# Performance work log

Measured on AMD Instinct MI355X. Metric: run time of the kernel, lower is better.

Reference implementation:

```python
import jax, jax.numpy as jnp
import numpy as np

B, T, C, K, V = 4, 4096, 128, 64, 64
EPS = 1e-5


def layer_norm(x, g, b):
    mu = jnp.mean(x, axis=-1, keepdims=True)
    var = jnp.var(x, axis=-1, keepdims=True)
    return (x - mu) * jax.lax.rsqrt(var + EPS) * g + b


def setup_inputs() -> dict:
    key = jax.random.key(0)
    ks = jax.random.split(key, 8)
    s = 1.0 / np.sqrt(C)
    return {
        "x": jax.random.normal(ks[0], (B, T, C), dtype=jnp.float32),
        "Wq": jax.random.uniform(ks[1], (C, K), jnp.float32, -s, s),
        "bq": jnp.zeros((K,), jnp.float32),
        "Wk": jax.random.uniform(ks[2], (C, K), jnp.float32, -s, s),
        "bk": jnp.zeros((K,), jnp.float32),
        "Wv": jax.random.uniform(ks[3], (C, V), jnp.float32, -s, s),
        "bv": jnp.zeros((V,), jnp.float32),
        "gq": jnp.ones((K,), jnp.float32), "bgq": jnp.zeros((K,), jnp.float32),
        "gk": jnp.ones((K,), jnp.float32), "bgk": jnp.zeros((K,), jnp.float32),
        "gv": jnp.ones((V,), jnp.float32), "bgv": jnp.zeros((V,), jnp.float32),
        "go": jnp.ones((V,), jnp.float32), "bgo": jnp.zeros((V,), jnp.float32),
    }


def reference(x, Wq, bq, Wk, bk, Wv, bv, gq, bgq, gk, bgk, gv, bgv, go, bgo):
    # projections: B x T x {K,K,V}
    q = layer_norm(x @ Wq + bq, gq, bgq)
    k = layer_norm(x @ Wk + bk, gk, bgk)
    v = layer_norm(x @ Wv + bv, gv, bgv)
    sqrt_k = jnp.asarray(np.sqrt(K), x.dtype)
    # full B x T x T causal score matrix (faithful to the original bmm+mask)
    logits = jnp.einsum("btk,bsk->bts", q, k) / sqrt_k
    t = jnp.arange(T)
    causal = t[:, None] >= t[None, :]  # lower-triangular incl. diagonal
    logits = jnp.where(causal[None], logits, -jnp.inf)
    probs = jax.nn.softmax(logits, axis=-1)
    read = jnp.einsum("bts,bsv->btv", probs, v)
    read = layer_norm(read, go, bgo)
    return jnp.concatenate([x, read], axis=2)  # B x T x (C+V)
```

## Files before the change

kernel.cpp:

```cpp
#include <hip/hip_runtime.h>

#define TT 4096

typedef unsigned short u16;
typedef unsigned int u32;

typedef short bf16x8 __attribute__((ext_vector_type(8)));
typedef float f32x4 __attribute__((ext_vector_type(4)));

union U8 {
  uint2 q[2];
  uint4 u4;
  bf16x8 v;
  short s[8];
};

static __device__ __forceinline__ u16 f2bf(float f) {
  union { float f; u32 u; } cv;
  cv.f = f;
  u32 r = cv.u + 0x7FFFu + ((cv.u >> 16) & 1u);
  return (u16)(r >> 16);
}
static __device__ __forceinline__ u32 pk2(float a, float b) {
  return (u32)f2bf(a) | ((u32)f2bf(b) << 16);
}
static __device__ __forceinline__ float bf2f(u16 h) {
  union { u32 u; float f; } cv;
  cv.u = ((u32)h) << 16;
  return cv.f;
}

__global__ __launch_bounds__(64)
void wpack(const float* __restrict__ Wq, const float* __restrict__ Wk,
           const float* __restrict__ Wv, u16* __restrict__ wf)
{
  const int g = blockIdx.x;
  const int p = g >> 4, s = (g >> 2) & 3, nt = g & 3;
  const int l = threadIdx.x, lg = l >> 4, l15 = l & 15;
  const float* W = (p == 0) ? Wq : (p == 1) ? Wk : Wv;
  const int n = l15 + 16 * nt;
  U8 o;
#pragma unroll
  for (int j = 0; j < 8; ++j) {
    int k = 32 * s + ((j < 4) ? (4 * lg + j) : (16 + 4 * lg + (j - 4)));
    o.s[j] = (short)f2bf(W[k * 64 + n]);
  }
  *(uint4*)(wf + (size_t)(g * 64 + l) * 8) = o.u4;
}

__global__ __launch_bounds__(256)
void proj_mfma(const float* __restrict__ x, const u16* __restrict__ wf,
               const float* __restrict__ bq, const float* __restrict__ bk,
               const float* __restrict__ bv,
               const float* __restrict__ gq, const float* __restrict__ bgq,
               const float* __restrict__ gk, const float* __restrict__ bgk,
               const float* __restrict__ gv, const float* __restrict__ bgv,
               u16* __restrict__ qo, u16* __restrict__ ko, u16* __restrict__ vto,
               float* __restrict__ out)
{
  __shared__ u16 xs[64 * 128];
  const int bx = blockIdx.x;
  const int xcd = bx & 7, i = bx >> 3;
  const int tile = xcd * 32 + (i & 31);
  const int p = i >> 5;
  const int rowbase = tile * 64;
  const int t = threadIdx.x;

  {
    const int row = t >> 2, seg = t & 3;
    const float4* src = (const float4*)(x + (size_t)(rowbase + row) * 128 + seg * 32);
    float4 f[8];
#pragma unroll
    for (int q = 0; q < 8; ++q) f[q] = src[q];
    if ((p == 0 && seg < 2) || (p == 1 && seg >= 2)) {
      float4* dst = (float4*)(out + (size_t)(rowbase + row) * 192 + seg * 32);
#pragma unroll
      for (int q = 0; q < 8; ++q) dst[q] = f[q];
    }
    const int base = row * 256 + seg * 64;
    const int swz = (row & 7) << 4;
    char* xb = (char*)xs;
#pragma unroll
    for (int q = 0; q < 4; ++q) {
      uint4 u;
      u.x = pk2(f[2 * q].x, f[2 * q].y);
      u.y = pk2(f[2 * q].z, f[2 * q].w);
      u.z = pk2(f[2 * q + 1].x, f[2 * q + 1].y);
      u.w = pk2(f[2 * q + 1].z, f[2 * q + 1].w);
      *(uint4*)(xb + ((base + 16 * q) ^ swz)) = u;
    }
  }

  const int w = t >> 6, l = t & 63, lg = l >> 4, l15 = l & 15;
  U8 bfr[4][4];
  const u16* wp = wf + (size_t)p * (16 * 64 * 8);
#pragma unroll
  for (int s = 0; s < 4; ++s)
#pragma unroll
    for (int nt = 0; nt < 4; ++nt)
      bfr[s][nt].u4 = *(const uint4*)(wp + ((s * 4 + nt) * 64 + l) * 8);

  __syncthreads();

  f32x4 acc[4];
#pragma unroll
  for (int nt = 0; nt < 4; ++nt) acc[nt] = (f32x4){0.f, 0.f, 0.f, 0.f};
  const int abase = (16 * w + l15) * 256;
  const int aswz = (l15 & 7) << 4;
  const char* xb = (const char*)xs;
#pragma unroll
  for (int s = 0; s < 4; ++s) {
    U8 af;
    af.q[0] = *(const uint2*)(xb + ((abase + s * 64 + 8 * lg) ^ aswz));
    af.q[1] = *(const uint2*)(xb + ((abase + s * 64 + 8 * lg + 32) ^ aswz));
#pragma unroll
    for (int nt = 0; nt < 4; ++nt)
      acc[nt] = __builtin_amdgcn_mfma_f32_16x16x32_bf16(af.v, bfr[s][nt].v, acc[nt], 0, 0, 0);
  }

  const float* bb = (p == 0) ? bq : (p == 1) ? bk : bv;
  const float* gg = (p == 0) ? gq : (p == 1) ? gk : gv;
  const float* hh = (p == 0) ? bgq : (p == 1) ? bgk : bgv;
  float bcol[4], gcol[4], hcol[4];
#pragma unroll
  for (int nt = 0; nt < 4; ++nt) {
    int col = l15 + 16 * nt;
    bcol[nt] = bb[col]; gcol[nt] = gg[col]; hcol[nt] = hh[col];
  }
  float vals[4][4];
#pragma unroll
  for (int nt = 0; nt < 4; ++nt)
#pragma unroll
    for (int r = 0; r < 4; ++r) vals[nt][r] = acc[nt][r] + bcol[nt];

  float s1[4], s2[4];
#pragma unroll
  for (int r = 0; r < 4; ++r) {
    s1[r] = vals[0][r] + vals[1][r] + vals[2][r] + vals[3][r];
    s2[r] = vals[0][r] * vals[0][r] + vals[1][r] * vals[1][r]
          + vals[2][r] * vals[2][r] + vals[3][r] * vals[3][r];
#pragma unroll
    for (int d = 1; d < 16; d <<= 1) {
      s1[r] += __shfl_xor(s1[r], d);
      s2[r] += __shfl_xor(s2[r], d);
    }
  }

  if (p < 2) {
    u16* dst = (p == 0) ? qo : ko;
#pragma unroll
    for (int r = 0; r < 4; ++r) {
      float mu = s1[r] * (1.f / 64.f);
      float var = s2[r] * (1.f / 64.f) - mu * mu;
      float rs = rsqrtf(var + 1e-5f);
      int grow = rowbase + 16 * w + 4 * lg + r;
#pragma unroll
      for (int nt = 0; nt < 4; ++nt)
        dst[(size_t)grow * 64 + l15 + 16 * nt] =
            f2bf((vals[nt][r] - mu) * rs * gcol[nt] + hcol[nt]);
    }
  } else {
    const int b = rowbase >> 12;
    const int tl0 = (rowbase & 4095) + 16 * w + 4 * lg;
#pragma unroll
    for (int r = 0; r < 4; ++r) {
      float mu = s1[r] * (1.f / 64.f);
      float var = s2[r] * (1.f / 64.f) - mu * mu;
      float rs = rsqrtf(var + 1e-5f);
#pragma unroll
      for (int nt = 0; nt < 4; ++nt)
        vto[(size_t)(b * 64 + l15 + 16 * nt) * TT + tl0 + r] =
            f2bf((vals[nt][r] - mu) * rs * gcol[nt] + hcol[nt]);
    }
  }
}

__global__ __launch_bounds__(256)
void attn_splitW(const u16* __restrict__ qg, const u16* __restrict__ kg,
                 const u16* __restrict__ vtg,
                 float* __restrict__ mP, float* __restrict__ lP,
                 u16* __restrict__ aP,
                 int Wseg, int maxseg, int halfcnt)
{
  __shared__ u16 kl[64 * 64];
  __shared__ u16 vl[64 * 64];
  const int bx = blockIdx.x;
  const int xcd = bx & 7, b = xcd >> 1, e = xcd & 1;
  const int j = e * halfcnt + (bx >> 3);
  const int Wh = Wseg >> 1;
  int Q = 0;
  while (Wh * (Q + 1) * (Q + 2) <= j) ++Q;
  const int ip = j - Wh * Q * (Q + 1);
  const int dv = ip / (Q + 1);
  const int q = Wseg * Q + dv;
  const int s = ip - dv * (Q + 1);
  const int q0 = q * 64;
  const int tileid = b * 64 + q;
  const int it0 = s * Wseg;
  const int it1 = min(it0 + Wseg, q + 1);

  const int t = threadIdx.x;
  const int w = t >> 6, l = t & 63;
  const int l15 = l & 15, lg = l >> 4;
  const int swzl = (l15 & 7) << 4;

  const int qrow = q0 + 16 * w + l15;
  const u16* qrp = qg + (size_t)(b * TT + qrow) * 64;
  U8 qf[2];
#pragma unroll
  for (int hh = 0; hh < 2; ++hh) {
    qf[hh].q[0] = *(const uint2*)(qrp + 32 * hh + 4 * lg);
    qf[hh].q[1] = *(const uint2*)(qrp + 32 * hh + 4 * lg + 16);
  }

  const int key = t >> 2;
  const int part = t & 3;
  const int sbase = key * 128 + part * 32;
  const int ssw = (key & 7) << 4;
  uint4 kr0, kr1, vr0, vr1;
  {
    const u16* ks = kg + (size_t)(b * TT + it0 * 64 + key) * 64 + part * 16;
    kr0 = ((const uint4*)ks)[0];
    kr1 = ((const uint4*)ks)[1];
    const u16* vs = vtg + (size_t)(b * 64 + key) * TT + it0 * 64 + part * 16;
    vr0 = ((const uint4*)vs)[0];
    vr1 = ((const uint4*)vs)[1];
  }

  float m_run = -1e30f, l_run = 0.f;
  f32x4 acc[4];
#pragma unroll
  for (int ct = 0; ct < 4; ++ct) acc[ct] = (f32x4){0.f, 0.f, 0.f, 0.f};

  for (int it = it0; it < it1; ++it) {
    const int kb = it * 64;
    {
      char* kd = (char*)kl;
      char* vd = (char*)vl;
      *(uint4*)(kd + ((sbase + 0) ^ ssw)) = kr0;
      *(uint4*)(kd + ((sbase + 16) ^ ssw)) = kr1;
      *(uint4*)(vd + ((sbase + 0) ^ ssw)) = vr0;
      *(uint4*)(vd + ((sbase + 16) ^ ssw)) = vr1;
    }
    __syncthreads();
    if (it + 1 < it1) {
      const u16* ks = kg + (size_t)(b * TT + (it + 1) * 64 + key) * 64 + part * 16;
      kr0 = ((const uint4*)ks)[0];
      kr1 = ((const uint4*)ks)[1];
      const u16* vs = vtg + (size_t)(b * 64 + key) * TT + (it + 1) * 64 + part * 16;
      vr0 = ((const uint4*)vs)[0];
      vr1 = ((const uint4*)vs)[1];
    }

    f32x4 st[4];
#pragma unroll
    for (int t4 = 0; t4 < 4; ++t4) {
      const int rbase = (16 * t4 + l15) * 128 + 8 * lg;
      const char* kp = (const char*)kl;
      U8 kf0, kf1;
      kf0.q[0] = *(const uint2*)(kp + ((rbase + 0) ^ swzl));
      kf0.q[1] = *(const uint2*)(kp + ((rbase + 32) ^ swzl));
      kf1.q[0] = *(const uint2*)(kp + ((rbase + 64) ^ swzl));
      kf1.q[1] = *(const uint2*)(kp + ((rbase + 96) ^ swzl));
      f32x4 d = {0.f, 0.f, 0.f, 0.f};
      d = __builtin_amdgcn_mfma_f32_16x16x32_bf16(kf0.v, qf[0].v, d, 0, 0, 0);
      d = __builtin_amdgcn_mfma_f32_16x16x32_bf16(kf1.v, qf[1].v, d, 0, 0, 0);
      st[t4] = d;
    }

    float sv[16];
    const bool needmask = (kb + 63 > q0 + 16 * w);
#pragma unroll
    for (int t4 = 0; t4 < 4; ++t4) {
#pragma unroll
      for (int r = 0; r < 4; ++r) {
        float sc = st[t4][r] * 0.125f;
        if (needmask) {
          int keyidx = kb + 16 * t4 + 4 * lg + r;
          if (keyidx > qrow) sc = -1e30f;
        }
        sv[t4 * 4 + r] = sc;
      }
    }
    float mt = sv[0];
#pragma unroll
    for (int i = 1; i < 16; ++i) mt = fmaxf(mt, sv[i]);
    mt = fmaxf(mt, __shfl_xor(mt, 16));
    mt = fmaxf(mt, __shfl_xor(mt, 32));
    const float mnew = fmaxf(m_run, mt);
    const float al = __expf(m_run - mnew);
    float pv[16];
    float rsum = 0.f;
#pragma unroll
    for (int i = 0; i < 16; ++i) { pv[i] = __expf(sv[i] - mnew); rsum += pv[i]; }
    rsum += __shfl_xor(rsum, 16);
    rsum += __shfl_xor(rsum, 32);
    l_run = l_run * al + rsum;
    m_run = mnew;
    float ar[4];
#pragma unroll
    for (int r = 0; r < 4; ++r) ar[r] = __shfl(al, 4 * lg + r);
#pragma unroll
    for (int ct = 0; ct < 4; ++ct) {
#pragma unroll
      for (int r = 0; r < 4; ++r) acc[ct][r] *= ar[r];
    }
    U8 pa[2];
#pragma unroll
    for (int u = 0; u < 2; ++u) {
#pragma unroll
      for (int i = 0; i < 8; ++i) pa[u].s[i] = (short)f2bf(pv[8 * u + i]);
    }

#pragma unroll
    for (int ct = 0; ct < 4; ++ct) {
      const int vb = (16 * ct + l15) * 128 + 8 * lg;
      const char* vp = (const char*)vl;
#pragma unroll
      for (int u = 0; u < 2; ++u) {
        U8 vf;
        vf.q[0] = *(const uint2*)(vp + ((vb + 64 * u + 0) ^ swzl));
        vf.q[1] = *(const uint2*)(vp + ((vb + 64 * u + 32) ^ swzl));
        acc[ct] = __builtin_amdgcn_mfma_f32_16x16x32_bf16(pa[u].v, vf.v, acc[ct], 0, 0, 0);
      }
    }
    __syncthreads();
  }

  const size_t pbase = (size_t)(tileid * maxseg + s) * 64;
  if (lg == 0) {
    mP[pbase + 16 * w + l15] = m_run;
    lP[pbase + 16 * w + l15] = l_run;
  }
#pragma unroll
  for (int ct = 0; ct < 4; ++ct) {
#pragma unroll
    for (int r = 0; r < 4; ++r) {
      int rin = 16 * w + 4 * lg + r;
      aP[(pbase + rin) * 64 + l15 + 16 * ct] = f2bf(acc[ct][r]);
    }
  }
}

__global__ __launch_bounds__(256)
void attn_mergeW(const float* __restrict__ mP, const float* __restrict__ lP,
                 const u16* __restrict__ aP,
                 const float* __restrict__ go, const float* __restrict__ bgo,
                 float* __restrict__ out, int jshift, int maxseg)
{
  const int t = threadIdx.x;
  const int w = t >> 6, c = t & 63;
  const int row = blockIdx.x * 4 + w;
  const int tid2 = row >> 6, rin = row & 63;
  const int q = tid2 & 63;
  const int ns = (q >> jshift) + 1;

  float m = -1e30f, L = 0.f, o = 0.f;
  for (int s = 0; s < ns; ++s) {
    const size_t pbase = (size_t)(tid2 * maxseg + s) * 64;
    float ms = mP[pbase + rin];
    float ls = lP[pbase + rin];
    float a = bf2f(aP[(pbase + rin) * 64 + c]);
    float mn = fmaxf(m, ms);
    float w0 = __expf(m - mn), w1 = __expf(ms - mn);
    L = L * w0 + ls * w1;
    o = o * w0 + a * w1;
    m = mn;
  }
  o /= L;

  float s1 = o, s2 = o * o;
#pragma unroll
  for (int d = 1; d < 64; d <<= 1) {
    s1 += __shfl_xor(s1, d);
    s2 += __shfl_xor(s2, d);
  }
  float mu = s1 * (1.f / 64.f);
  float var = s2 * (1.f / 64.f) - mu * mu;
  float rs = rsqrtf(var + 1e-5f);
  out[(size_t)row * 192 + 128 + c] = (o - mu) * rs * go[c] + bgo[c];
}

__global__ __launch_bounds__(128)
void attn1(const u16* __restrict__ qg, const u16* __restrict__ kg,
           const u16* __restrict__ vtg,
           const float* __restrict__ go, const float* __restrict__ bgo,
           float* __restrict__ out)
{
  __shared__ u16 kl[64 * 64];
  __shared__ u16 vl[64 * 64];
  const int bx = blockIdx.x;
  const int tt = (bx < 256) ? bx : (767 - bx);
  const int b = tt >> 7;
  const int q0 = (tt & 127) * 32;
  const int tid = threadIdx.x;
  const int w = tid >> 6;
  const int l = tid & 63;
  const int l15 = l & 15;
  const int lg = l >> 4;
  const int swzl = (l15 & 7) << 4;

  const int qrow = q0 + 16 * w + l15;
  const u16* qrp = qg + (size_t)(b * TT + qrow) * 64;
  U8 qf[2];
#pragma unroll
  for (int h = 0; h < 2; ++h) {
    qf[h].q[0] = *(const uint2*)(qrp + 32 * h + 4 * lg);
    qf[h].q[1] = *(const uint2*)(qrp + 32 * h + 4 * lg + 16);
  }

  float m_run = -1e30f, l_run = 0.f;
  f32x4 acc[4];
#pragma unroll
  for (int ct = 0; ct < 4; ++ct) acc[ct] = (f32x4){0.f, 0.f, 0.f, 0.f};

  const int nkv = (q0 >> 6) + 1;
  for (int it = 0; it < nkv; ++it) {
    const int kb = it * 64;
    {
      const int key = tid >> 1;
      const int dh = (tid & 1) * 32;
      const u16* ks = kg + (size_t)(b * TT + kb + key) * 64 + dh;
      uint4 d0 = *(const uint4*)(ks + 0);
      uint4 d1 = *(const uint4*)(ks + 8);
      uint4 d2 = *(const uint4*)(ks + 16);
      uint4 d3 = *(const uint4*)(ks + 24);
      const int base = key * 128 + dh * 2;
      const int sw = (key & 7) << 4;
      char* kd = (char*)kl;
      *(uint4*)(kd + ((base + 0) ^ sw)) = d0;
      *(uint4*)(kd + ((base + 16) ^ sw)) = d1;
      *(uint4*)(kd + ((base + 32) ^ sw)) = d2;
      *(uint4*)(kd + ((base + 48) ^ sw)) = d3;
      const u16* vs = vtg + (size_t)(b * 64 + key) * TT + kb + dh;
      uint4 e0 = *(const uint4*)(vs + 0);
      uint4 e1 = *(const uint4*)(vs + 8);
      uint4 e2 = *(const uint4*)(vs + 16);
      uint4 e3 = *(const uint4*)(vs + 24);
      char* vd = (char*)vl;
      *(uint4*)(vd + ((base + 0) ^ sw)) = e0;
      *(uint4*)(vd + ((base + 16) ^ sw)) = e1;
      *(uint4*)(vd + ((base + 32) ^ sw)) = e2;
      *(uint4*)(vd + ((base + 48) ^ sw)) = e3;
    }
    __syncthreads();

    f32x4 st[4];
#pragma unroll
    for (int t4 = 0; t4 < 4; ++t4) {
      const int rbase = (16 * t4 + l15) * 128 + 8 * lg;
      const char* kp = (const char*)kl;
      U8 kf0, kf1;
      kf0.q[0] = *(const uint2*)(kp + ((rbase + 0) ^ swzl));
      kf0.q[1] = *(const uint2*)(kp + ((rbase + 32) ^ swzl));
      kf1.q[0] = *(const uint2*)(kp + ((rbase + 64) ^ swzl));
      kf1.q[1] = *(const uint2*)(kp + ((rbase + 96) ^ swzl));
      f32x4 d = {0.f, 0.f, 0.f, 0.f};
      d = __builtin_amdgcn_mfma_f32_16x16x32_bf16(kf0.v, qf[0].v, d, 0, 0, 0);
      d = __builtin_amdgcn_mfma_f32_16x16x32_bf16(kf1.v, qf[1].v, d, 0, 0, 0);
      st[t4] = d;
    }

    float sv[16];
    const bool needmask = (kb + 63 > q0 + 16 * w);
#pragma unroll
    for (int t4 = 0; t4 < 4; ++t4) {
#pragma unroll
      for (int r = 0; r < 4; ++r) {
        float sc = st[t4][r] * 0.125f;
        if (needmask) {
          int keyidx = kb + 16 * t4 + 4 * lg + r;
          if (keyidx > qrow) sc = -1e30f;
        }
        sv[t4 * 4 + r] = sc;
      }
    }
    float mt = sv[0];
#pragma unroll
    for (int i = 1; i < 16; ++i) mt = fmaxf(mt, sv[i]);
    mt = fmaxf(mt, __shfl_xor(mt, 16));
    mt = fmaxf(mt, __shfl_xor(mt, 32));
    const float mnew = fmaxf(m_run, mt);
    const float al = __expf(m_run - mnew);
    float p[16];
    float rsum = 0.f;
#pragma unroll
    for (int i = 0; i < 16; ++i) { p[i] = __expf(sv[i] - mnew); rsum += p[i]; }
    rsum += __shfl_xor(rsum, 16);
    rsum += __shfl_xor(rsum, 32);
    l_run = l_run * al + rsum;
    m_run = mnew;
    float ar[4];
#pragma unroll
    for (int r = 0; r < 4; ++r) ar[r] = __shfl(al, 4 * lg + r);
#pragma unroll
    for (int ct = 0; ct < 4; ++ct) {
#pragma unroll
      for (int r = 0; r < 4; ++r) acc[ct][r] *= ar[r];
    }
    U8 pa[2];
#pragma unroll
    for (int u = 0; u < 2; ++u) {
#pragma unroll
      for (int i = 0; i < 8; ++i) pa[u].s[i] = (short)f2bf(p[8 * u + i]);
    }

#pragma unroll
    for (int ct = 0; ct < 4; ++ct) {
      const int vb = (16 * ct + l15) * 128 + 8 * lg;
      const char* vp = (const char*)vl;
#pragma unroll
      for (int u = 0; u < 2; ++u) {
        U8 vf;
        vf.q[0] = *(const uint2*)(vp + ((vb + 64 * u + 0) ^ swzl));
        vf.q[1] = *(const uint2*)(vp + ((vb + 64 * u + 32) ^ swzl));
        acc[ct] = __builtin_amdgcn_mfma_f32_16x16x32_bf16(pa[u].v, vf.v, acc[ct], 0, 0, 0);
      }
    }
    __syncthreads();
  }

  float linv[4];
#pragma unroll
  for (int r = 0; r < 4; ++r) linv[r] = 1.f / __shfl(l_run, 4 * lg + r);
  float o[4][4];
#pragma unroll
  for (int ct = 0; ct < 4; ++ct) {
#pragma unroll
    for (int r = 0; r < 4; ++r) o[ct][r] = acc[ct][r] * linv[r];
  }
  float s1[4], s2[4];
#pragma unroll
  for (int r = 0; r < 4; ++r) {
    s1[r] = o[0][r] + o[1][r] + o[2][r] + o[3][r];
    s2[r] = o[0][r] * o[0][r] + o[1][r] * o[1][r] + o[2][r] * o[2][r] + o[3][r] * o[3][r];
#pragma unroll
    for (int d = 1; d < 16; d <<= 1) {
      s1[r] += __shfl_xor(s1[r], d);
      s2[r] += __shfl_xor(s2[r], d);
    }
  }
  float gov[4], bgv2[4];
#pragma unroll
  for (int ct = 0; ct < 4; ++ct) {
    gov[ct] = go[16 * ct + l15];
    bgv2[ct] = bgo[16 * ct + l15];
  }
#pragma unroll
  for (int r = 0; r < 4; ++r) {
    float mu = s1[r] * (1.f / 64.f);
    float var = s2[r] * (1.f / 64.f) - mu * mu;
    float rs = rsqrtf(var + 1e-5f);
    int row = q0 + 16 * w + 4 * lg + r;
    float* op = out + (size_t)(b * TT + row) * 192 + 128;
#pragma unroll
    for (int ct = 0; ct < 4; ++ct)
      op[16 * ct + l15] = (o[ct][r] - mu) * rs * gov[ct] + bgv2[ct];
  }
}

extern "C" void kernel_launch(void* const* d_in, const int* in_sizes, int n_in,
                              void* d_out, int out_size, void* d_ws, size_t ws_size,
                              hipStream_t stream) {
  (void)in_sizes; (void)n_in; (void)out_size;
  const float* x   = (const float*)d_in[0];
  const float* Wq  = (const float*)d_in[1];
  const float* bq  = (const float*)d_in[2];
  const float* Wk  = (const float*)d_in[3];
  const float* bk  = (const float*)d_in[4];
  const float* Wv  = (const float*)d_in[5];
  const float* bv  = (const float*)d_in[6];
  const float* gq  = (const float*)d_in[7];
  const float* bgq = (const float*)d_in[8];
  const float* gk  = (const float*)d_in[9];
  const float* bgk = (const float*)d_in[10];
  const float* gv  = (const float*)d_in[11];
  const float* bgv = (const float*)d_in[12];
  const float* go  = (const float*)d_in[13];
  const float* bgo = (const float*)d_in[14];
  float* out = (float*)d_out;

  char* wsb = (char*)d_ws;
  u16* qws  = (u16*)wsb;
  u16* kws  = (u16*)(wsb + (2u << 20));
  u16* vtws = (u16*)(wsb + (4u << 20));
  u16* wfr  = (u16*)(wsb + (6u << 20));
  const size_t OFF_MP = (6u << 20) + 65536;

  wpack<<<48, 64, 0, stream>>>(Wq, Wk, Wv, wfr);
  proj_mfma<<<768, 256, 0, stream>>>(x, wfr, bq, bk, bv,
                                     gq, bgq, gk, bgk, gv, bgv,
                                     qws, kws, vtws, out);

  {
    const size_t MPS8 = 256u * 8 * 64 * 4;
    const size_t APS8 = 256u * 8 * 64 * 64 * 2;
    const size_t OFF_LP8 = OFF_MP + MPS8;
    const size_t OFF_AP8 = OFF_LP8 + MPS8;
    const size_t NEED8 = OFF_AP8 + APS8;
    const size_t MPS32 = 256u * 2 * 64 * 4;
    const size_t APS32 = 256u * 2 * 64 * 64 * 2;
    const size_t OFF_LP32 = OFF_MP + MPS32;
    const size_t OFF_AP32 = OFF_LP32 + MPS32;
    const size_t NEED32 = OFF_AP32 + APS32;

    if (ws_size >= NEED8) {
      float* mP = (float*)(wsb + OFF_MP);
      float* lP = (float*)(wsb + OFF_LP8);
      u16*   aP = (u16*)(wsb + OFF_AP8);
      attn_splitW<<<1152, 256, 0, stream>>>(qws, kws, vtws, mP, lP, aP, 8, 8, 144);
      attn_mergeW<<<4096, 256, 0, stream>>>(mP, lP, aP, go, bgo, out, 3, 8);
    } else if (ws_size >= NEED32) {
      float* mP = (float*)(wsb + OFF_MP);
      float* lP = (float*)(wsb + OFF_LP32);
      u16*   aP = (u16*)(wsb + OFF_AP32);
      attn_splitW<<<384, 256, 0, stream>>>(qws, kws, vtws, mP, lP, aP, 32, 2, 48);
      attn_mergeW<<<4096, 256, 0, stream>>>(mP, lP, aP, go, bgo, out, 5, 2);
    } else {
      attn1<<<512, 128, 0, stream>>>(qws, kws, vtws, go, bgo, out);
    }
  }
}
```

Measured before the change: 72.40 us.

## Load K/V MFMA fragments directly from global, drop LDS staging and barriers

The split-attention kernel no longer stages K and V tiles through shared memory with swizzled writes and two __syncthreads per iteration. Each wave now loads its K and V MFMA fragments straight from global memory, relying on the caches to absorb the fourfold redundant reads across waves. The softmax also moves to the base-2 domain: the log2(e)/8 factor is folded into the score scale and raw v_exp_f32 is used in both split and merge. It also adds a hardware bf16 pack instruction and tree-shaped max and sum reductions. The trade-off is more global and L1 traffic and the loss of the register prefetch of the next tile, in exchange for no LDS round trip and no block-wide synchronisation.

Measured after the change: 186.0 us. +156.9%, slower.

```diff
diff --git a/kernel.cpp b/kernel.cpp
--- a/kernel.cpp
+++ b/kernel.cpp
@@ -13,6 +13,7 @@
   uint4 u4;
   bf16x8 v;
   short s[8];
+  u32 w[4];
 };
 
 static __device__ __forceinline__ u16 f2bf(float f) {
@@ -28,6 +29,12 @@
   union { u32 u; float f; } cv;
   cv.u = ((u32)h) << 16;
   return cv.f;
+}
+static __device__ __forceinline__ float exp2a(float x) {
+  float r; asm("v_exp_f32 %0, %1" : "=v"(r) : "v"(x)); return r;
+}
+static __device__ __forceinline__ u32 cvtpk(float lo, float hi) {
+  u32 r; asm("v_cvt_pk_bf16_f32 %0, %1, %2" : "=v"(r) : "v"(lo), "v"(hi)); return r;
 }
 
 __global__ __launch_bounds__(64)
@@ -176,14 +183,12 @@
 }
 
 __global__ __launch_bounds__(256)
-void attn_splitW(const u16* __restrict__ qg, const u16* __restrict__ kg,
+void attn_splitD(const u16* __restrict__ qg, const u16* __restrict__ kg,
                  const u16* __restrict__ vtg,
                  float* __restrict__ mP, float* __restrict__ lP,
                  u16* __restrict__ aP,
                  int Wseg, int maxseg, int halfcnt)
 {
-  __shared__ u16 kl[64 * 64];
-  __shared__ u16 vl[64 * 64];
   const int bx = blockIdx.x;
   const int xcd = bx & 7, b = xcd >> 1, e = xcd & 1;
   const int j = e * halfcnt + (bx >> 3);
@@ -202,7 +207,6 @@
   const int t = threadIdx.x;
   const int w = t >> 6, l = t & 63;
   const int l15 = l & 15, lg = l >> 4;
-  const int swzl = (l15 & 7) << 4;
 
   const int qrow = q0 + 16 * w + l15;
   const u16* qrp = qg + (size_t)(b * TT + qrow) * 64;
@@ -213,19 +217,13 @@
     qf[hh].q[1] = *(const uint2*)(qrp + 32 * hh + 4 * lg + 16);
   }
 
-  const int key = t >> 2;
-  const int part = t & 3;
-  const int sbase = key * 128 + part * 32;
-  const int ssw = (key & 7) << 4;
-  uint4 kr0, kr1, vr0, vr1;
-  {
-    const u16* ks = kg + (size_t)(b * TT + it0 * 64 + key) * 64 + part * 16;
-    kr0 = ((const uint4*)ks)[0];
-    kr1 = ((const uint4*)ks)[1];
-    const u16* vs = vtg + (size_t)(b * 64 + key) * TT + it0 * 64 + part * 16;
-    vr0 = ((const uint4*)vs)[0];
-    vr1 = ((const uint4*)vs)[1];
-  }
+  const u16* kp = kg + (size_t)(b * TT + it0 * 64 + l15) * 64 + 4 * lg;
+  const u16* vp0 = vtg + (size_t)(b * 64 + l15) * TT + it0 * 64 + 4 * lg;
+  const u16* vp1 = vp0 + (size_t)16 * TT;
+  const u16* vp2 = vp0 + (size_t)32 * TT;
+  const u16* vp3 = vp0 + (size_t)48 * TT;
+
+  const float C = 0.18033688011112042f;
 
   float m_run = -1e30f, l_run = 0.f;
   f32x4 acc[4];
@@ -234,65 +232,77 @@
 
   for (int it = it0; it < it1; ++it) {
     const int kb = it * 64;
-    {
-      char* kd = (char*)kl;
-      char* vd = (char*)vl;
-      *(uint4*)(kd + ((sbase + 0) ^ ssw)) = kr0;
-      *(uint4*)(kd + ((sbase + 16) ^ ssw)) = kr1;
-      *(uint4*)(vd + ((sbase + 0) ^ ssw)) = vr0;
-      *(uint4*)(vd + ((sbase + 16) ^ ssw)) = vr1;
-    }
-    __syncthreads();
-    if (it + 1 < it1) {
-      const u16* ks = kg + (size_t)(b * TT + (it + 1) * 64 + key) * 64 + part * 16;
-      kr0 = ((const uint4*)ks)[0];
-      kr1 = ((const uint4*)ks)[1];
-      const u16* vs = vtg + (size_t)(b * 64 + key) * TT + (it + 1) * 64 + part * 16;
-      vr0 = ((const uint4*)vs)[0];
-      vr1 = ((const uint4*)vs)[1];
+
+    U8 kf[4][2];
+#pragma unroll
+    for (int t4 = 0; t4 < 4; ++t4) {
+#pragma unroll
+      for (int h = 0; h < 2; ++h) {
+        kf[t4][h].q[0] = *(const uint2*)(kp + t4 * 1024 + 32 * h);
+        kf[t4][h].q[1] = *(const uint2*)(kp + t4 * 1024 + 32 * h + 16);
+      }
     }
 
     f32x4 st[4];
 #pragma unroll
     for (int t4 = 0; t4 < 4; ++t4) {
-      const int rbase = (16 * t4 + l15) * 128 + 8 * lg;
-      const char* kp = (const char*)kl;
-      U8 kf0, kf1;
-      kf0.q[0] = *(const uint2*)(kp + ((rbase + 0) ^ swzl));
-      kf0.q[1] = *(const uint2*)(kp + ((rbase + 32) ^ swzl));
-      kf1.q[0] = *(const uint2*)(kp + ((rbase + 64) ^ swzl));
-      kf1.q[1] = *(const uint2*)(kp + ((rbase + 96) ^ swzl));
       f32x4 d = {0.f, 0.f, 0.f, 0.f};
-      d = __builtin_amdgcn_mfma_f32_16x16x32_bf16(kf0.v, qf[0].v, d, 0, 0, 0);
-      d = __builtin_amdgcn_mfma_f32_16x16x32_bf16(kf1.v, qf[1].v, d, 0, 0, 0);
+      d = __builtin_amdgcn_mfma_f32_16x16x32_bf16(kf[t4][0].v, qf[0].v, d, 0, 0, 0);
+      d = __builtin_amdgcn_mfma_f32_16x16x32_bf16(kf[t4][1].v, qf[1].v, d, 0, 0, 0);
       st[t4] = d;
+    }
+
+    U8 vf[4][2];
+#pragma unroll
+    for (int u = 0; u < 2; ++u) {
+      vf[0][u].q[0] = *(const uint2*)(vp0 + 32 * u);
+      vf[0][u].q[1] = *(const uint2*)(vp0 + 32 * u + 16);
+      vf[1][u].q[0] = *(const uint2*)(vp1 + 32 * u);
+      vf[1][u].q[1] = *(const uint2*)(vp1 + 32 * u + 16);
+      vf[2][u].q[0] = *(const uint2*)(vp2 + 32 * u);
+      vf[2][u].q[1] = *(const uint2*)(vp2 + 32 * u + 16);
+      vf[3][u].q[0] = *(const uint2*)(vp3 + 32 * u);
+      vf[3][u].q[1] = *(const uint2*)(vp3 + 32 * u + 16);
     }
 
     float sv[16];
     const bool needmask = (kb + 63 > q0 + 16 * w);
-#pragma unroll
-    for (int t4 = 0; t4 < 4; ++t4) {
-#pragma unroll
-      for (int r = 0; r < 4; ++r) {
-        float sc = st[t4][r] * 0.125f;
-        if (needmask) {
+    if (needmask) {
+#pragma unroll
+      for (int t4 = 0; t4 < 4; ++t4) {
+#pragma unroll
+        for (int r = 0; r < 4; ++r) {
+          float sc = st[t4][r] * C;
           int keyidx = kb + 16 * t4 + 4 * lg + r;
-          if (keyidx > qrow) sc = -1e30f;
+          sv[t4 * 4 + r] = (keyidx > qrow) ? -1e30f : sc;
         }
-        sv[t4 * 4 + r] = sc;
       }
-    }
-    float mt = sv[0];
-#pragma unroll
-    for (int i = 1; i < 16; ++i) mt = fmaxf(mt, sv[i]);
+    } else {
+#pragma unroll
+      for (int t4 = 0; t4 < 4; ++t4) {
+#pragma unroll
+        for (int r = 0; r < 4; ++r) sv[t4 * 4 + r] = st[t4][r] * C;
+      }
+    }
+    float mx[8];
+#pragma unroll
+    for (int i = 0; i < 8; ++i) mx[i] = fmaxf(sv[2 * i], sv[2 * i + 1]);
+#pragma unroll
+    for (int i = 0; i < 4; ++i) mx[i] = fmaxf(mx[2 * i], mx[2 * i + 1]);
+    float mt = fmaxf(fmaxf(mx[0], mx[1]), fmaxf(mx[2], mx[3]));
     mt = fmaxf(mt, __shfl_xor(mt, 16));
     mt = fmaxf(mt, __shfl_xor(mt, 32));
     const float mnew = fmaxf(m_run, mt);
-    const float al = __expf(m_run - mnew);
-    float pv[16];
-    float rsum = 0.f;
-#pragma unroll
-    for (int i = 0; i < 16; ++i) { pv[i] = __expf(sv[i] - mnew); rsum += pv[i]; }
+    const float al = exp2a(m_run - mnew);
+    float p[16];
+#pragma unroll
+    for (int i = 0; i < 16; ++i) p[i] = exp2a(sv[i] - mnew);
+    float sm[8];
+#pragma unroll
+    for (int i = 0; i < 8; ++i) sm[i] = p[2 * i] + p[2 * i + 1];
+#pragma unroll
+    for (int i = 0; i < 4; ++i) sm[i] = sm[2 * i] + sm[2 * i + 1];
+    float rsum = (sm[0] + sm[1]) + (sm[2] + sm[3]);
     rsum += __shfl_xor(rsum, 16);
     rsum += __shfl_xor(rsum, 32);
     l_run = l_run * al + rsum;
@@ -309,22 +319,19 @@
 #pragma unroll
     for (int u = 0; u < 2; ++u) {
 #pragma unroll
-      for (int i = 0; i < 8; ++i) pa[u].s[i] = (short)f2bf(pv[8 * u + i]);
+      for (int k2 = 0; k2 < 4; ++k2)
+        pa[u].w[k2] = cvtpk(p[8 * u + 2 * k2], p[8 * u + 2 * k2 + 1]);
     }
 
 #pragma unroll
     for (int ct = 0; ct < 4; ++ct) {
-      const int vb = (16 * ct + l15) * 128 + 8 * lg;
-      const char* vp = (const char*)vl;
-#pragma unroll
-      for (int u = 0; u < 2; ++u) {
-        U8 vf;
-        vf.q[0] = *(const uint2*)(vp + ((vb + 64 * u + 0) ^ swzl));
-        vf.q[1] = *(const uint2*)(vp + ((vb + 64 * u + 32) ^ swzl));
-        acc[ct] = __builtin_amdgcn_mfma_f32_16x16x32_bf16(pa[u].v, vf.v, acc[ct], 0, 0, 0);
-      }
-    }
-    __syncthreads();
+#pragma unroll
+      for (int u = 0; u < 2; ++u)
+        acc[ct] = __builtin_amdgcn_mfma_f32_16x16x32_bf16(pa[u].v, vf[ct][u].v, acc[ct], 0, 0, 0);
+    }
+
+    kp += 4096;
+    vp0 += 64; vp1 += 64; vp2 += 64; vp3 += 64;
   }
 
   const size_t pbase = (size_t)(tileid * maxseg + s) * 64;
@@ -362,7 +369,7 @@
     float ls = lP[pbase + rin];
     float a = bf2f(aP[(pbase + rin) * 64 + c]);
     float mn = fmaxf(m, ms);
-    float w0 = __expf(m - mn), w1 = __expf(ms - mn);
+    float w0 = exp2a(m - mn), w1 = exp2a(ms - mn);
     L = L * w0 + ls * w1;
     o = o * w0 + a * w1;
     m = mn;
@@ -608,13 +615,13 @@
       float* mP = (float*)(wsb + OFF_MP);
       float* lP = (float*)(wsb + OFF_LP8);
       u16*   aP = (u16*)(wsb + OFF_AP8);
-      attn_splitW<<<1152, 256, 0, stream>>>(qws, kws, vtws, mP, lP, aP, 8, 8, 144);
+      attn_splitD<<<1152, 256, 0, stream>>>(qws, kws, vtws, mP, lP, aP, 8, 8, 144);
       attn_mergeW<<<4096, 256, 0, stream>>>(mP, lP, aP, go, bgo, out, 3, 8);
     } else if (ws_size >= NEED32) {
       float* mP = (float*)(wsb + OFF_MP);
       float* lP = (float*)(wsb + OFF_LP32);
       u16*   aP = (u16*)(wsb + OFF_AP32);
-      attn_splitW<<<384, 256, 0, stream>>>(qws, kws, vtws, mP, lP, aP, 32, 2, 48);
+      attn_splitD<<<384, 256, 0, stream>>>(qws, kws, vtws, mP, lP, aP, 32, 2, 48);
       attn_mergeW<<<4096, 256, 0, stream>>>(mP, lP, aP, go, bgo, out, 5, 2);
     } else {
       attn1<<<512, 128, 0, stream>>>(qws, kws, vtws, go, bgo, out);
```

## Add fixed 4-tile split-K attention kernel with preloaded LDS and lazy rescale

Applied to the files above, without the earlier changes.

Adds a new attention path that splits each query tile's causal key range into segments of four 64-key tiles. Each block preloads all four K/V tiles into swizzled LDS with one barrier, then runs an online softmax. It uses hardware exp2 and packed bf16 conversion, and skips the accumulator rescale unless the max grows past a threshold. A matching merge kernel combines the per-segment partials and applies the output layernorm. This yields more, shorter blocks (2176) for better load balance and fewer syncs, at the cost of more partial-result traffic and a larger workspace.

After: 65.21 us. 1.11x faster.

```diff
diff --git a/kernel.cpp b/kernel.cpp
--- a/kernel.cpp
+++ b/kernel.cpp
@@ -13,6 +13,7 @@
   uint4 u4;
   bf16x8 v;
   short s[8];
+  u32 w[4];
 };
 
 static __device__ __forceinline__ u16 f2bf(float f) {
@@ -28,6 +29,12 @@
   union { u32 u; float f; } cv;
   cv.u = ((u32)h) << 16;
   return cv.f;
+}
+static __device__ __forceinline__ float exp2a(float x) {
+  float r; asm("v_exp_f32 %0, %1" : "=v"(r) : "v"(x)); return r;
+}
+static __device__ __forceinline__ u32 cvtpk(float lo, float hi) {
+  u32 r; asm("v_cvt_pk_bf16_f32 %0, %1, %2" : "=v"(r) : "v"(lo), "v"(hi)); return r;
 }
 
 __global__ __launch_bounds__(64)
@@ -173,6 +180,231 @@
             f2bf((vals[nt][r] - mu) * rs * gcol[nt] + hcol[nt]);
     }
   }
+}
+
+__global__ __launch_bounds__(256)
+void attn_seg4(const u16* __restrict__ qg, const u16* __restrict__ kg,
+               const u16* __restrict__ vtg,
+               float* __restrict__ mP, float* __restrict__ lP,
+               u16* __restrict__ aP)
+{
+  __shared__ u16 kl4[4 * 64 * 64];
+  __shared__ u16 vl4[4 * 64 * 64];
+  const int bx = blockIdx.x;
+  const int xcd = bx & 7, b = xcd >> 1, e = xcd & 1;
+  const int j = e * 272 + (bx >> 3);
+  int Q = 0;
+  while (2 * (Q + 1) * (Q + 2) <= j) ++Q;
+  const int ip = j - 2 * Q * (Q + 1);
+  const int dv = ip / (Q + 1);
+  const int q = 4 * Q + dv;
+  const int s = ip - dv * (Q + 1);
+  const int q0 = q * 64;
+  const int it0 = s * 4;
+  const int it1 = min(it0 + 4, q + 1);
+
+  const int t = threadIdx.x;
+  const int w = t >> 6, l = t & 63;
+  const int l15 = l & 15, lg = l >> 4;
+  const int swzl = (l15 & 7) << 4;
+
+  const int qrow = q0 + 16 * w + l15;
+  const u16* qrp = qg + (size_t)(b * TT + qrow) * 64;
+  U8 qf[2];
+#pragma unroll
+  for (int hh = 0; hh < 2; ++hh) {
+    qf[hh].q[0] = *(const uint2*)(qrp + 32 * hh + 4 * lg);
+    qf[hh].q[1] = *(const uint2*)(qrp + 32 * hh + 4 * lg + 16);
+  }
+
+  {
+    const int key = t >> 2, part = t & 3;
+    const int sbase = key * 128 + part * 32;
+    const int ssw = (key & 7) << 4;
+    uint4 kr[4][2], vr[4][2];
+#pragma unroll
+    for (int tt = 0; tt < 4; ++tt) {
+      int tile = it0 + tt; if (tile >= it1) tile = it1 - 1;
+      const u16* ks = kg + (size_t)(b * TT + tile * 64 + key) * 64 + part * 16;
+      kr[tt][0] = ((const uint4*)ks)[0];
+      kr[tt][1] = ((const uint4*)ks)[1];
+      const u16* vs = vtg + (size_t)(b * 64 + key) * TT + tile * 64 + part * 16;
+      vr[tt][0] = ((const uint4*)vs)[0];
+      vr[tt][1] = ((const uint4*)vs)[1];
+    }
+#pragma unroll
+    for (int tt = 0; tt < 4; ++tt) {
+      char* kd = (char*)kl4 + tt * 8192;
+      char* vd = (char*)vl4 + tt * 8192;
+      *(uint4*)(kd + ((sbase + 0) ^ ssw)) = kr[tt][0];
+      *(uint4*)(kd + ((sbase + 16) ^ ssw)) = kr[tt][1];
+      *(uint4*)(vd + ((sbase + 0) ^ ssw)) = vr[tt][0];
+      *(uint4*)(vd + ((sbase + 16) ^ ssw)) = vr[tt][1];
+    }
+  }
+  __syncthreads();
+
+  const float C = 0.18033688011112042f;
+  float m_run = -1e30f, l_run = 0.f;
+  f32x4 acc[4];
+#pragma unroll
+  for (int ct = 0; ct < 4; ++ct) acc[ct] = (f32x4){0.f, 0.f, 0.f, 0.f};
+
+  int toff = 0;
+  for (int it = it0; it < it1; ++it, toff += 8192) {
+    const int kb = it * 64;
+    const char* kp = (const char*)kl4 + toff;
+    const char* vp = (const char*)vl4 + toff;
+
+    f32x4 st[4];
+    __builtin_amdgcn_s_setprio(1);
+#pragma unroll
+    for (int t4 = 0; t4 < 4; ++t4) {
+      const int rbase = (16 * t4 + l15) * 128 + 8 * lg;
+      U8 kf0, kf1;
+      kf0.q[0] = *(const uint2*)(kp + ((rbase + 0) ^ swzl));
+      kf0.q[1] = *(const uint2*)(kp + ((rbase + 32) ^ swzl));
+      kf1.q[0] = *(const uint2*)(kp + ((rbase + 64) ^ swzl));
+      kf1.q[1] = *(const uint2*)(kp + ((rbase + 96) ^ swzl));
+      f32x4 d = {0.f, 0.f, 0.f, 0.f};
+      d = __builtin_amdgcn_mfma_f32_16x16x32_bf16(kf0.v, qf[0].v, d, 0, 0, 0);
+      d = __builtin_amdgcn_mfma_f32_16x16x32_bf16(kf1.v, qf[1].v, d, 0, 0, 0);
+      st[t4] = d;
+    }
+    __builtin_amdgcn_s_setprio(0);
+
+    float sv[16];
+    const bool needmask = (kb + 63 > q0 + 16 * w);
+    if (needmask) {
+#pragma unroll
+      for (int t4 = 0; t4 < 4; ++t4) {
+#pragma unroll
+        for (int r = 0; r < 4; ++r) {
+          float sc = st[t4][r] * C;
+          int keyidx = kb + 16 * t4 + 4 * lg + r;
+          sv[t4 * 4 + r] = (keyidx > qrow) ? -1e30f : sc;
+        }
+      }
+    } else {
+#pragma unroll
+      for (int t4 = 0; t4 < 4; ++t4) {
+#pragma unroll
+        for (int r = 0; r < 4; ++r) sv[t4 * 4 + r] = st[t4][r] * C;
+      }
+    }
+    float mx[8];
+#pragma unroll
+    for (int i = 0; i < 8; ++i) mx[i] = fmaxf(sv[2 * i], sv[2 * i + 1]);
+#pragma unroll
+    for (int i = 0; i < 4; ++i) mx[i] = fmaxf(mx[2 * i], mx[2 * i + 1]);
+    float mt = fmaxf(fmaxf(mx[0], mx[1]), fmaxf(mx[2], mx[3]));
+    mt = fmaxf(mt, __shfl_xor(mt, 16));
+    mt = fmaxf(mt, __shfl_xor(mt, 32));
+
+    if (!__all(mt - m_run <= 11.5f)) {
+      const float mnew = fmaxf(m_run, mt);
+      const float al = exp2a(m_run - mnew);
+      l_run *= al;
+      float ar[4];
+#pragma unroll
+      for (int r = 0; r < 4; ++r) ar[r] = __shfl(al, 4 * lg + r);
+#pragma unroll
+      for (int ct = 0; ct < 4; ++ct) {
+#pragma unroll
+        for (int r = 0; r < 4; ++r) acc[ct][r] *= ar[r];
+      }
+      m_run = mnew;
+    }
+    float p[16];
+#pragma unroll
+    for (int i = 0; i < 16; ++i) p[i] = exp2a(sv[i] - m_run);
+    float sm[8];
+#pragma unroll
+    for (int i = 0; i < 8; ++i) sm[i] = p[2 * i] + p[2 * i + 1];
+#pragma unroll
+    for (int i = 0; i < 4; ++i) sm[i] = sm[2 * i] + sm[2 * i + 1];
+    float rsum = (sm[0] + sm[1]) + (sm[2] + sm[3]);
+    rsum += __shfl_xor(rsum, 16);
+    rsum += __shfl_xor(rsum, 32);
+    l_run += rsum;
+
+    U8 pa[2];
+#pragma unroll
+    for (int u = 0; u < 2; ++u) {
+#pragma unroll
+      for (int k2 = 0; k2 < 4; ++k2)
+        pa[u].w[k2] = cvtpk(p[8 * u + 2 * k2], p[8 * u + 2 * k2 + 1]);
+    }
+
+    __builtin_amdgcn_s_setprio(1);
+#pragma unroll
+    for (int ct = 0; ct < 4; ++ct) {
+      const int vb = (16 * ct + l15) * 128 + 8 * lg;
+#pragma unroll
+      for (int u = 0; u < 2; ++u) {
+        U8 vf;
+        vf.q[0] = *(const uint2*)(vp + ((vb + 64 * u + 0) ^ swzl));
+        vf.q[1] = *(const uint2*)(vp + ((vb + 64 * u + 32) ^ swzl));
+        acc[ct] = __builtin_amdgcn_mfma_f32_16x16x32_bf16(pa[u].v, vf.v, acc[ct], 0, 0, 0);
+      }
+    }
+    __builtin_amdgcn_s_setprio(0);
+  }
+
+  const size_t pbase = (size_t)(b * 544 + j) * 64;
+  if (lg == 0) {
+    mP[pbase + 16 * w + l15] = m_run;
+    lP[pbase + 16 * w + l15] = l_run;
+  }
+#pragma unroll
+  for (int ct = 0; ct < 4; ++ct) {
+#pragma unroll
+    for (int r = 0; r < 4; ++r) {
+      int rin = 16 * w + 4 * lg + r;
+      aP[(pbase + rin) * 64 + l15 + 16 * ct] = f2bf(acc[ct][r]);
+    }
+  }
+}
+
+__global__ __launch_bounds__(256)
+void attn_merge4(const float* __restrict__ mP, const float* __restrict__ lP,
+                 const u16* __restrict__ aP,
+                 const float* __restrict__ go, const float* __restrict__ bgo,
+                 float* __restrict__ out)
+{
+  const int t = threadIdx.x;
+  const int w = t >> 6, c = t & 63;
+  const int row = blockIdx.x * 4 + w;
+  const int tid2 = row >> 6, rin = row & 63;
+  const int b = tid2 >> 6, q = tid2 & 63;
+  const int Q = q >> 2;
+  const int base_q = b * 544 + 2 * Q * (Q + 1) + (q & 3) * (Q + 1);
+  const int ns = Q + 1;
+
+  float m = -1e30f, L = 0.f, o = 0.f;
+  for (int s = 0; s < ns; ++s) {
+    const size_t pb = (size_t)(base_q + s) * 64;
+    float ms = mP[pb + rin];
+    float ls = lP[pb + rin];
+    float a = bf2f(aP[(pb + rin) * 64 + c]);
+    float mn = fmaxf(m, ms);
+    float w0 = exp2a(m - mn), w1 = exp2a(ms - mn);
+    L = L * w0 + ls * w1;
+    o = o * w0 + a * w1;
+    m = mn;
+  }
+  o /= L;
+
+  float s1 = o, s2 = o * o;
+#pragma unroll
+  for (int d = 1; d < 64; d <<= 1) {
+    s1 += __shfl_xor(s1, d);
+    s2 += __shfl_xor(s2, d);
+  }
+  float mu = s1 * (1.f / 64.f);
+  float var = s2 * (1.f / 64.f) - mu * mu;
+  float rs = rsqrtf(var + 1e-5f);
+  out[(size_t)row * 192 + 128 + c] = (o - mu) * rs * go[c] + bgo[c];
 }
 
 __global__ __launch_bounds__(256)
@@ -593,6 +825,12 @@
                                      qws, kws, vtws, out);
 
   {
+    const size_t SEG4 = 4u * 544;
+    const size_t MPS4 = SEG4 * 64 * 4;
+    const size_t APS4 = SEG4 * 64 * 64 * 2;
+    const size_t OFF_LP4 = OFF_MP + MPS4;
+    const size_t OFF_AP4 = OFF_LP4 + MPS4;
+    const size_t NEED4 = OFF_AP4 + APS4;
     const size_t MPS8 = 256u * 8 * 64 * 4;
     const size_t APS8 = 256u * 8 * 64 * 64 * 2;
     const size_t OFF_LP8 = OFF_MP + MPS8;
@@ -604,7 +842,13 @@
     const size_t OFF_AP32 = OFF_LP32 + MPS32;
     const size_t NEED32 = OFF_AP32 + APS32;
 
-    if (ws_size >= NEED8) {
+    if (ws_size >= NEED4) {
+      float* mP = (float*)(wsb + OFF_MP);
+      float* lP = (float*)(wsb + OFF_LP4);
+      u16*   aP = (u16*)(wsb + OFF_AP4);
+      attn_seg4<<<2176, 256, 0, stream>>>(qws, kws, vtws, mP, lP, aP);
+      attn_merge4<<<4096, 256, 0, stream>>>(mP, lP, aP, go, bgo, out);
+    } else if (ws_size >= NEED8) {
       float* mP = (float*)(wsb + OFF_MP);
       float* lP = (float*)(wsb + OFF_LP8);
       u16*   aP = (u16*)(wsb + OFF_AP8);
```
